# Performance work log

Measured on AMD Instinct MI355X. Metric: run time of the kernel, lower is better.

The kernel has to match this reference:

```python
import jax, jax.numpy as jnp
import numpy as np

FACTOR = 5

def setup_inputs() -> dict:
    key = jax.random.key(0)
    k1, k2, k3, k4 = jax.random.split(key, 4)
    B, L, H, D = 4, 4096, 8, 64
    sample_k = min(FACTOR * int(np.ceil(np.log(L))), L)  # 45
    queries = jax.random.normal(k1, (B, L, H, D), jnp.float32)
    keys = jax.random.normal(k2, (B, L, H, D), jnp.float32)
    values = jax.random.normal(k3, (B, L, H, D), jnp.float32)
    # torch.randint(L_K, (L_Q, sample_k)) hoisted here for determinism
    index_sample = jax.random.randint(k4, (L, sample_k), 0, L, dtype=jnp.int32)
    return {"queries": queries, "keys": keys, "values": values,
            "index_sample": index_sample}


def reference(queries, keys, values, index_sample):
    B, L_Q, H, D = queries.shape
    L_K = keys.shape[1]
    # [B,L,H,D] -> [B,H,L,D]
    Q = jnp.transpose(queries, (0, 2, 1, 3))
    K = jnp.transpose(keys, (0, 2, 1, 3))
    V = jnp.transpose(values, (0, 2, 1, 3))

    u = min(FACTOR * int(np.ceil(np.log(L_Q))), L_Q)  # n_top queries

    # --- _prob_QK: sampled QK, sparsity measure, top-u query selection ---
    # K_sample[b,h,q,s,:] = K[b,h,index_sample[q,s],:]
    K_sample = K[:, :, index_sample, :]                        # [B,H,L_Q,Sk,D]
    Q_K_sample = jnp.einsum('bhqd,bhqsd->bhqs', Q, K_sample)   # [B,H,L_Q,Sk]
    M = Q_K_sample.max(axis=-1) - Q_K_sample.sum(axis=-1) / L_K
    _, M_top = jax.lax.top_k(M, u)                             # [B,H,u]

    Q_reduce = jnp.take_along_axis(Q, M_top[..., None], axis=2)  # [B,H,u,D]
    scale = 1.0 / np.sqrt(D).astype(np.float32)
    scores = jnp.einsum('bhud,bhkd->bhuk', Q_reduce, K) * scale  # [B,H,u,L_K]

    # --- masked causal attention on the selected rows (mask_flag=True) ---
    # ProbMask: triu(1) rows gathered at M_top -> mask where col > query pos
    causal_mask = M_top[..., None] < jnp.arange(L_K)             # [B,H,u,L_K]
    scores = jnp.where(causal_mask, -jnp.inf, scores)
    attn = jax.nn.softmax(scores, axis=-1)

    # --- initial context (masked => cumsum of V), scatter top-u updates ---
    context = jnp.cumsum(V, axis=2)                              # [B,H,L_Q,D]
    update = jnp.einsum('bhuk,bhkd->bhud', attn, V)              # [B,H,u,D]
    b_idx = jnp.arange(B)[:, None, None]
    h_idx = jnp.arange(H)[None, :, None]
    context = context.at[b_idx, h_idx, M_top].set(update)
    return context  # [B,H,L_Q,D]
```

## Files before the change

### kernel.cpp

```cpp
#include <hip/hip_runtime.h>
#include <float.h>
#include <math.h>

#define B_ 4
#define L_ 4096
#define H_ 8
#define D_ 64
#define S_ 45
#define KC_ 16
#define KCH_ 256
#define SCALE 0.125f

typedef __attribute__((ext_vector_type(8))) short short8;
typedef __attribute__((ext_vector_type(4))) float float4v;

__device__ __forceinline__ ushort f2bf(float x) {
  unsigned u = __float_as_uint(x);
  return (ushort)((u + 0x7FFFu + ((u >> 16) & 1u)) >> 16);
}

__device__ __forceinline__ int swz_us(int row, int col_b, int rowb, int m) {
  int slot = (col_b >> 4) ^ (row & m);
  return row * (rowb >> 1) + (slot << 3) + ((col_b & 15) >> 1);
}

__global__ __launch_bounds__(256) void kA(
    const float* __restrict__ Q, const float* __restrict__ K,
    const float* __restrict__ V, const int* __restrict__ idxs,
    float* __restrict__ M, float* __restrict__ cs)
{
  int blk = blockIdx.x;
  int grp = blk / 136, within = blk % 136;
  int tid = threadIdx.x;
  int w = tid >> 6, lane = tid & 63;

  if (within >= 128) {
    int cblk = grp * 8 + (within - 128);
    int bh = cblk >> 4, cg = cblk & 15;
    int b = bh >> 3, h = bh & 7;
    int t = lane & 15, rg = lane >> 4;
    int c = cg * 4 + w;
    int l0 = c * 64;
    const float4* V4 = (const float4*)V;
    float4 acc = make_float4(0.f, 0.f, 0.f, 0.f);
    for (int step = 0; step < 16; ++step) {
      int l = l0 + step * 4 + rg;
      float4 v = V4[((size_t)(b * L_ + l) * H_ + h) * 16 + t];
      acc.x += v.x; acc.y += v.y; acc.z += v.z; acc.w += v.w;
    }
    acc.x += __shfl_xor(acc.x, 16, 64); acc.y += __shfl_xor(acc.y, 16, 64);
    acc.z += __shfl_xor(acc.z, 16, 64); acc.w += __shfl_xor(acc.w, 16, 64);
    acc.x += __shfl_xor(acc.x, 32, 64); acc.y += __shfl_xor(acc.y, 32, 64);
    acc.z += __shfl_xor(acc.z, 32, 64); acc.w += __shfl_xor(acc.w, 32, 64);
    if (rg == 0)
      ((float4*)cs)[((size_t)bh * 64 + c) * 16 + t] = acc;
    return;
  }

  int kblk = grp * 128 + within;
  int g = kblk & 7;
  int chunk = kblk >> 3;
  int b = g >> 1, hh = g & 1;
  int t = lane & 15;
  int l = chunk * 4 + w;

  const float4* qp = (const float4*)(Q + ((size_t)(b * L_ + l) * H_ + hh * 4) * D_);
  float4 qv = qp[lane];

  int s = lane < S_ ? lane : S_ - 1;
  int idxall = idxs[l * S_ + s];

  float vmax = -FLT_MAX, vsum = 0.f;
  #pragma unroll
  for (int c = 0; c < 5; ++c) {
    int kidx[9];
    #pragma unroll
    for (int j = 0; j < 9; ++j) kidx[j] = __shfl(idxall, c * 9 + j, 64);
    float4 kv[9];
    #pragma unroll
    for (int j = 0; j < 9; ++j) {
      const float4* kp =
          (const float4*)(K + ((size_t)(b * L_ + kidx[j]) * H_ + hh * 4) * D_);
      kv[j] = kp[lane];
    }
    #pragma unroll
    for (int j = 0; j < 9; ++j) {
      float p = qv.x * kv[j].x;
      p = fmaf(qv.y, kv[j].y, p);
      p = fmaf(qv.z, kv[j].z, p);
      p = fmaf(qv.w, kv[j].w, p);
      p += __shfl_xor(p, 1, 64);
      p += __shfl_xor(p, 2, 64);
      p += __shfl_xor(p, 4, 64);
      p += __shfl_xor(p, 8, 64);
      vmax = fmaxf(vmax, p);
      vsum += p;
    }
  }
  if (t == 0) {
    int h = hh * 4 + (lane >> 4);
    M[(size_t)(b * H_ + h) * L_ + l] = vmax - vsum * (1.0f / L_);
  }
}

__device__ __forceinline__ unsigned ordf(float f) {
  unsigned u = __float_as_uint(f);
  return (u & 0x80000000u) ? ~u : (u | 0x80000000u);
}

__global__ __launch_bounds__(256) void kB(
    const float* __restrict__ M, int* __restrict__ mtop, float* __restrict__ cs)
{
  int blk = blockIdx.x;
  int tid = threadIdx.x;
  if (blk >= 32) {
    int g = (blk - 32) * 256 + tid;
    int bh = g >> 6, d = g & 63;
    float run = 0.f;
    for (int c = 0; c < 64; ++c) {
      size_t off = ((size_t)bh * 64 + c) * D_ + d;
      float a = cs[off];
      cs[off] = run;
      run += a;
    }
    return;
  }
  __shared__ unsigned long long cand[4][S_];
  int bh = blk;
  int w = tid >> 6, lane = tid & 63;
  const float* Mp = M + (size_t)bh * L_;
  unsigned long long key[16];
  #pragma unroll
  for (int j = 0; j < 16; ++j) {
    int gi = w * 1024 + j * 64 + lane;
    key[j] = ((unsigned long long)ordf(Mp[gi]) << 32) | (unsigned)(~gi);
  }
  for (int it = 0; it < S_; ++it) {
    unsigned long long loc = key[0];
    #pragma unroll
    for (int j = 1; j < 16; ++j) loc = key[j] > loc ? key[j] : loc;
    unsigned long long best = loc;
    #pragma unroll
    for (int m = 32; m >= 1; m >>= 1) {
      unsigned long long o = __shfl_xor(best, m, 64);
      best = o > best ? o : best;
    }
    if (loc == best) {
      #pragma unroll
      for (int j = 0; j < 16; ++j) if (key[j] == best) key[j] = 0ull;
    }
    if (lane == 0) cand[w][it] = best;
  }
  __syncthreads();
  if (w == 0) {
    unsigned long long k2[3];
    #pragma unroll
    for (int j = 0; j < 3; ++j) {
      int c = j * 64 + lane;
      k2[j] = (c < 4 * S_) ? cand[c / S_][c % S_] : 0ull;
    }
    for (int it = 0; it < S_; ++it) {
      unsigned long long loc = k2[0];
      loc = k2[1] > loc ? k2[1] : loc;
      loc = k2[2] > loc ? k2[2] : loc;
      unsigned long long best = loc;
      #pragma unroll
      for (int m = 32; m >= 1; m >>= 1) {
        unsigned long long o = __shfl_xor(best, m, 64);
        best = o > best ? o : best;
      }
      if (loc == best) {
        #pragma unroll
        for (int j = 0; j < 3; ++j) if (k2[j] == best) k2[j] = 0ull;
      }
      if (lane == 0) mtop[bh * S_ + it] = (int)(~(unsigned)(best & 0xFFFFFFFFu));
    }
  }
}

__global__ __launch_bounds__(256) void kATT(
    const float* __restrict__ Q, const float* __restrict__ K,
    const float* __restrict__ V, const int* __restrict__ mtop,
    float* __restrict__ lpart, float* __restrict__ updp)
{
  __shared__ __align__(16) ushort Ks[256 * 64];
  __shared__ __align__(16) ushort Qs[48 * 64];
  __shared__ __align__(16) ushort Ps[48 * 256];
  __shared__ float lred[4][48];
  __shared__ int   cut[48];

  int blk = blockIdx.x;
  int kc = blk >> 5;
  int r5 = blk & 31;
  int bh = ((r5 & 7) << 2) | (r5 >> 3);
  int b = bh >> 3, h = bh & 7;
  int tid = threadIdx.x;
  int w = tid >> 6, lane = tid & 63;
  int l15 = lane & 15, l4 = lane >> 4;

  if (tid < 48) cut[tid] = (tid < S_) ? mtop[bh * S_ + tid] : -1;
  __syncthreads();

  {
    const float4* kp =
        (const float4*)(K + ((size_t)(b * L_ + kc * KCH_ + tid) * H_ + h) * D_);
    #pragma unroll
    for (int c = 0; c < 8; ++c) {
      float4 a = kp[2 * c], bb = kp[2 * c + 1];
      uint4 pk;
      pk.x = f2bf(a.x) | ((unsigned)f2bf(a.y) << 16);
      pk.y = f2bf(a.z) | ((unsigned)f2bf(a.w) << 16);
      pk.z = f2bf(bb.x) | ((unsigned)f2bf(bb.y) << 16);
      pk.w = f2bf(bb.z) | ((unsigned)f2bf(bb.w) << 16);
      *(uint4*)&Ks[swz_us(tid, c * 16, 128, 7)] = pk;
    }
  }
  for (int i = tid; i < 48 * 8; i += 256) {
    int row = i >> 3, c = i & 7;
    uint4 pk = make_uint4(0, 0, 0, 0);
    if (row < S_) {
      const float4* qp =
          (const float4*)(Q + ((size_t)(b * L_ + cut[row]) * H_ + h) * D_);
      float4 a = qp[2 * c], bb = qp[2 * c + 1];
      pk.x = f2bf(a.x) | ((unsigned)f2bf(a.y) << 16);
      pk.y = f2bf(a.z) | ((unsigned)f2bf(a.w) << 16);
      pk.z = f2bf(bb.x) | ((unsigned)f2bf(bb.y) << 16);
      pk.w = f2bf(bb.z) | ((unsigned)f2bf(bb.w) << 16);
    }
    *(uint4*)&Qs[swz_us(row, c * 16, 128, 7)] = pk;
  }
  __syncthreads();

  float4v accS[3][4];
  #pragma unroll
  for (int mt = 0; mt < 3; ++mt)
    #pragma unroll
    for (int nt = 0; nt < 4; ++nt)
      accS[mt][nt] = (float4v){0.f, 0.f, 0.f, 0.f};
  #pragma unroll
  for (int ks = 0; ks < 2; ++ks) {
    short8 afr[3];
    #pragma unroll
    for (int mt = 0; mt < 3; ++mt)
      afr[mt] = *(const short8*)&Qs[swz_us(mt * 16 + l15, ks * 64 + l4 * 16, 128, 7)];
    #pragma unroll
    for (int nt = 0; nt < 4; ++nt) {
      short8 bfr = *(const short8*)
          &Ks[swz_us(w * 64 + nt * 16 + l15, ks * 64 + l4 * 16, 128, 7)];
      #pragma unroll
      for (int mt = 0; mt < 3; ++mt)
        accS[mt][nt] = __builtin_amdgcn_mfma_f32_16x16x32_bf16(
            afr[mt], bfr, accS[mt][nt], 0, 0, 0);
    }
  }

  #pragma unroll
  for (int mt = 0; mt < 3; ++mt) {
    #pragma unroll
    for (int j = 0; j < 4; ++j) {
      int row = mt * 16 + l4 * 4 + j;
      int ct = cut[row];
      float rs = 0.f;
      #pragma unroll
      for (int nt = 0; nt < 4; ++nt) {
        int col = w * 64 + nt * 16 + l15;
        int kg = kc * KCH_ + col;
        float e = (kg <= ct) ? __expf(accS[mt][nt][j] * SCALE) : 0.f;
        rs += e;
        Ps[swz_us(row, col * 2, 512, 15)] = f2bf(e);
      }
      rs += __shfl_xor(rs, 1, 64);
      rs += __shfl_xor(rs, 2, 64);
      rs += __shfl_xor(rs, 4, 64);
      rs += __shfl_xor(rs, 8, 64);
      if (l15 == 0) lred[w][row] = rs;
    }
  }
  __syncthreads();

  if (tid < S_)
    lpart[((size_t)(bh * KC_ + kc)) * S_ + tid] =
        lred[0][tid] + lred[1][tid] + lred[2][tid] + lred[3][tid];

  {
    const float4* vp =
        (const float4*)(V + ((size_t)(b * L_ + kc * KCH_ + tid) * H_ + h) * D_);
    #pragma unroll
    for (int c = 0; c < 16; ++c) {
      float4 v = vp[c];
      int d0 = c * 4;
      Ks[swz_us(d0 + 0, tid * 2, 512, 15)] = f2bf(v.x);
      Ks[swz_us(d0 + 1, tid * 2, 512, 15)] = f2bf(v.y);
      Ks[swz_us(d0 + 2, tid * 2, 512, 15)] = f2bf(v.z);
      Ks[swz_us(d0 + 3, tid * 2, 512, 15)] = f2bf(v.w);
    }
  }
  __syncthreads();

  float4v accU[3];
  #pragma unroll
  for (int i = 0; i < 3; ++i) accU[i] = (float4v){0.f, 0.f, 0.f, 0.f};
  #pragma unroll
  for (int ks = 0; ks < 8; ++ks) {
    #pragma unroll
    for (int i = 0; i < 3; ++i) {
      int pi = w * 3 + i, mt = pi >> 2, nt = pi & 3;
      short8 afr = *(const short8*)
          &Ps[swz_us(mt * 16 + l15, ks * 64 + l4 * 16, 512, 15)];
      short8 bfr = *(const short8*)
          &Ks[swz_us(nt * 16 + l15, ks * 64 + l4 * 16, 512, 15)];
      accU[i] = __builtin_amdgcn_mfma_f32_16x16x32_bf16(afr, bfr, accU[i], 0, 0, 0);
    }
  }
  float* up = updp + ((size_t)(bh * KC_ + kc)) * (S_ * D_);
  #pragma unroll
  for (int i = 0; i < 3; ++i) {
    int pi = w * 3 + i, mt = pi >> 2, nt = pi & 3;
    #pragma unroll
    for (int j = 0; j < 4; ++j) {
      int row = mt * 16 + l4 * 4 + j;
      if (row < S_) up[row * D_ + nt * 16 + l15] = accU[i][j];
    }
  }
}

__global__ __launch_bounds__(256) void kW(
    const float* __restrict__ V, const float* __restrict__ cs,
    float* __restrict__ out)
{
  int blk = blockIdx.x;
  int bh = blk >> 4, cg = blk & 15;
  int b = bh >> 3, h = bh & 7;
  int w = threadIdx.x >> 6, lane = threadIdx.x & 63;
  int t = lane & 15, rg = lane >> 4;
  int c = cg * 4 + w;
  int l0 = c * 64;
  const float4* V4 = (const float4*)V;
  float4* O4 = (float4*)out;
  float4 carry = ((const float4*)cs)[((size_t)bh * 64 + c) * 16 + t];
  for (int step = 0; step < 16; ++step) {
    int l = l0 + step * 4 + rg;
    float4 v = V4[((size_t)(b * L_ + l) * H_ + h) * 16 + t];
    float4 u;
    u.x = __shfl_up(v.x, 16, 64); u.y = __shfl_up(v.y, 16, 64);
    u.z = __shfl_up(v.z, 16, 64); u.w = __shfl_up(v.w, 16, 64);
    if (rg >= 1) { v.x += u.x; v.y += u.y; v.z += u.z; v.w += u.w; }
    u.x = __shfl_up(v.x, 32, 64); u.y = __shfl_up(v.y, 32, 64);
    u.z = __shfl_up(v.z, 32, 64); u.w = __shfl_up(v.w, 32, 64);
    if (rg >= 2) { v.x += u.x; v.y += u.y; v.z += u.z; v.w += u.w; }
    float4 o;
    o.x = carry.x + v.x; o.y = carry.y + v.y;
    o.z = carry.z + v.z; o.w = carry.w + v.w;
    O4[((size_t)bh * L_ + l) * 16 + t] = o;
    carry.x += __shfl(v.x, 48 + t, 64); carry.y += __shfl(v.y, 48 + t, 64);
    carry.z += __shfl(v.z, 48 + t, 64); carry.w += __shfl(v.w, 48 + t, 64);
  }
}

__global__ __launch_bounds__(256) void kD(
    const float* __restrict__ lpart, const float* __restrict__ updp,
    const int* __restrict__ mtop, float* __restrict__ out)
{
  __shared__ float linv[S_];
  __shared__ int   mt[S_];
  int bh = blockIdx.x;
  int tid = threadIdx.x;
  if (tid < S_) {
    float l = 0.f;
    for (int kc = 0; kc < KC_; ++kc) l += lpart[(size_t)(bh * KC_ + kc) * S_ + tid];
    linv[tid] = 1.0f / l;
    mt[tid] = mtop[bh * S_ + tid];
  }
  __syncthreads();
  for (int i = tid; i < S_ * D_; i += 256) {
    int r = i >> 6, d = i & 63;
    float u = 0.f;
    for (int kc = 0; kc < KC_; ++kc) u += updp[((size_t)(bh * KC_ + kc)) * (S_ * D_) + i];
    out[((size_t)bh * L_ + mt[r]) * D_ + d] = u * linv[r];
  }
}

extern "C" void kernel_launch(void* const* d_in, const int* in_sizes, int n_in,
                              void* d_out, int out_size, void* d_ws, size_t ws_size,
                              hipStream_t stream) {
  const float* Q = (const float*)d_in[0];
  const float* K = (const float*)d_in[1];
  const float* V = (const float*)d_in[2];
  const int*   I = (const int*)d_in[3];
  float* out = (float*)d_out;
  float* ws = (float*)d_ws;

  float* M     = ws;
  float* cs    = ws + 131072;
  float* lpart = ws + 262144;
  float* updp  = ws + 262144 + 23040;
  int*   mtop  = (int*)(ws + 262144 + 23040 + 1474560);

  kA<<<64 * 136, 256, 0, stream>>>(Q, K, V, I, M, cs);
  kB<<<40, 256, 0, stream>>>(M, mtop, cs);
  kATT<<<B_ * H_ * KC_, 256, 0, stream>>>(Q, K, V, mtop, lpart, updp);
  kW<<<B_ * H_ * 16, 256, 0, stream>>>(V, cs, out);
  kD<<<B_ * H_, 256, 0, stream>>>(lpart, updp, mtop, out);
}
```

Baseline: 188.0 us.

## Fuse cumsum writer into attention kernel and halve key chunk size

Merges the cumsum-writer kernel into the attention kernel as extra block roles, interleaving 8 writer blocks with 16 attention blocks per group. It also halves the key chunk to 128, doubling the attention blocks to 1024 and using less shared memory each. The kB prefix scan now loads its 64 values into registers before writing them back. The aim is more parallelism and occupancy and one fewer launch, at the cost of twice the partial sums, so kD does more reduction work.

```diff
diff --git a/kernel.cpp b/kernel.cpp
--- a/kernel.cpp
+++ b/kernel.cpp
@@ -7,8 +7,8 @@
 #define H_ 8
 #define D_ 64
 #define S_ 45
-#define KC_ 16
-#define KCH_ 256
+#define KC2_ 32
+#define KCH2_ 128
 #define SCALE 0.125f
 
 typedef __attribute__((ext_vector_type(8))) short short8;
@@ -116,11 +116,14 @@
   if (blk >= 32) {
     int g = (blk - 32) * 256 + tid;
     int bh = g >> 6, d = g & 63;
+    float v[64];
+    #pragma unroll
+    for (int c = 0; c < 64; ++c) v[c] = cs[((size_t)bh * 64 + c) * D_ + d];
     float run = 0.f;
+    #pragma unroll
     for (int c = 0; c < 64; ++c) {
-      size_t off = ((size_t)bh * 64 + c) * D_ + d;
-      float a = cs[off];
-      cs[off] = run;
+      float a = v[c];
+      cs[((size_t)bh * 64 + c) * D_ + d] = run;
       run += a;
     }
     return;
@@ -178,41 +181,77 @@
   }
 }
 
-__global__ __launch_bounds__(256) void kATT(
+__global__ __launch_bounds__(256) void kCW(
     const float* __restrict__ Q, const float* __restrict__ K,
-    const float* __restrict__ V, const int* __restrict__ mtop,
-    float* __restrict__ lpart, float* __restrict__ updp)
+    const float* __restrict__ V, const float* __restrict__ cs,
+    const int* __restrict__ mtop, float* __restrict__ lpart,
+    float* __restrict__ updp, float* __restrict__ out)
 {
-  __shared__ __align__(16) ushort Ks[256 * 64];
+  __shared__ __align__(16) ushort Ks[128 * 64];
   __shared__ __align__(16) ushort Qs[48 * 64];
-  __shared__ __align__(16) ushort Ps[48 * 256];
+  __shared__ __align__(16) ushort Ps[48 * 128];
   __shared__ float lred[4][48];
   __shared__ int   cut[48];
 
   int blk = blockIdx.x;
-  int kc = blk >> 5;
-  int r5 = blk & 31;
+  int grp = blk / 24, within = blk % 24;
+  int tid = threadIdx.x;
+  int w = tid >> 6, lane = tid & 63;
+
+  if (within >= 16) {
+    int wblk = grp * 8 + (within - 16);
+    int bh = wblk >> 4, cg = wblk & 15;
+    int b = bh >> 3, h = bh & 7;
+    int t = lane & 15, rg = lane >> 4;
+    int c = cg * 4 + w;
+    int l0 = c * 64;
+    const float4* V4 = (const float4*)V;
+    float4* O4 = (float4*)out;
+    float4 carry = ((const float4*)cs)[((size_t)bh * 64 + c) * 16 + t];
+    for (int step = 0; step < 16; ++step) {
+      int l = l0 + step * 4 + rg;
+      float4 v = V4[((size_t)(b * L_ + l) * H_ + h) * 16 + t];
+      float4 u;
+      u.x = __shfl_up(v.x, 16, 64); u.y = __shfl_up(v.y, 16, 64);
+      u.z = __shfl_up(v.z, 16, 64); u.w = __shfl_up(v.w, 16, 64);
+      if (rg >= 1) { v.x += u.x; v.y += u.y; v.z += u.z; v.w += u.w; }
+      u.x = __shfl_up(v.x, 32, 64); u.y = __shfl_up(v.y, 32, 64);
+      u.z = __shfl_up(v.z, 32, 64); u.w = __shfl_up(v.w, 32, 64);
+      if (rg >= 2) { v.x += u.x; v.y += u.y; v.z += u.z; v.w += u.w; }
+      float4 o;
+      o.x = carry.x + v.x; o.y = carry.y + v.y;
+      o.z = carry.z + v.z; o.w = carry.w + v.w;
+      O4[((size_t)bh * L_ + l) * 16 + t] = o;
+      carry.x += __shfl(v.x, 48 + t, 64); carry.y += __shfl(v.y, 48 + t, 64);
+      carry.z += __shfl(v.z, 48 + t, 64); carry.w += __shfl(v.w, 48 + t, 64);
+    }
+    return;
+  }
+
+  int ablk = grp * 16 + within;
+  int kc = ablk >> 5;
+  int r5 = ablk & 31;
   int bh = ((r5 & 7) << 2) | (r5 >> 3);
   int b = bh >> 3, h = bh & 7;
-  int tid = threadIdx.x;
-  int w = tid >> 6, lane = tid & 63;
   int l15 = lane & 15, l4 = lane >> 4;
 
   if (tid < 48) cut[tid] = (tid < S_) ? mtop[bh * S_ + tid] : -1;
   __syncthreads();
 
   {
+    int row = tid & 127, half = tid >> 7;
     const float4* kp =
-        (const float4*)(K + ((size_t)(b * L_ + kc * KCH_ + tid) * H_ + h) * D_);
-    #pragma unroll
-    for (int c = 0; c < 8; ++c) {
+        (const float4*)(K + ((size_t)(b * L_ + kc * KCH2_ + row) * H_ + h) * D_);
+    #pragma unroll
+    for (int cc = 0; cc < 4; ++cc) {
+      int c = half * 4 + cc;
       float4 a = kp[2 * c], bb = kp[2 * c + 1];
       uint4 pk;
       pk.x = f2bf(a.x) | ((unsigned)f2bf(a.y) << 16);
       pk.y = f2bf(a.z) | ((unsigned)f2bf(a.w) << 16);
       pk.z = f2bf(bb.x) | ((unsigned)f2bf(bb.y) << 16);
       pk.w = f2bf(bb.z) | ((unsigned)f2bf(bb.w) << 16);
-      *(uint4*)&Ks[swz_us(tid, c * 16, 128, 7)] = pk;
+      *(uint4*)&Ks[swz_us(row, c * 16, 128, 7)] = pk;
     }
   }
   for (int i = tid; i < 48 * 8; i += 256) {
@@ -231,11 +270,11 @@
   }
   __syncthreads();
 
-  float4v accS[3][4];
+  float4v accS[3][2];
   #pragma unroll
   for (int mt = 0; mt < 3; ++mt)
     #pragma unroll
-    for (int nt = 0; nt < 4; ++nt)
+    for (int nt = 0; nt < 2; ++nt)
       accS[mt][nt] = (float4v){0.f, 0.f, 0.f, 0.f};
   #pragma unroll
   for (int ks = 0; ks < 2; ++ks) {
@@ -244,9 +283,9 @@
     for (int mt = 0; mt < 3; ++mt)
       afr[mt] = *(const short8*)&Qs[swz_us(mt * 16 + l15, ks * 64 + l4 * 16, 128, 7)];
     #pragma unroll
-    for (int nt = 0; nt < 4; ++nt) {
+    for (int nt = 0; nt < 2; ++nt) {
       short8 bfr = *(const short8*)
-          &Ks[swz_us(w * 64 + nt * 16 + l15, ks * 64 + l4 * 16, 128, 7)];
+          &Ks[swz_us(w * 32 + nt * 16 + l15, ks * 64 + l4 * 16, 128, 7)];
       #pragma unroll
       for (int mt = 0; mt < 3; ++mt)
         accS[mt][nt] = __builtin_amdgcn_mfma_f32_16x16x32_bf16(
@@ -262,12 +301,12 @@
       int ct = cut[row];
       float rs = 0.f;
       #pragma unroll
-      for (int nt = 0; nt < 4; ++nt) {
-        int col = w * 64 + nt * 16 + l15;
-        int kg = kc * KCH_ + col;
+      for (int nt = 0; nt < 2; ++nt) {
+        int col = w * 32 + nt * 16 + l15;
+        int kg = kc * KCH2_ + col;
         float e = (kg <= ct) ? __expf(accS[mt][nt][j] * SCALE) : 0.f;
         rs += e;
-        Ps[swz_us(row, col * 2, 512, 15)] = f2bf(e);
+        Ps[swz_us(row, col * 2, 256, 15)] = f2bf(e);
       }
       rs += __shfl_xor(rs, 1, 64);
       rs += __shfl_xor(rs, 2, 64);
@@ -279,20 +318,22 @@
   __syncthreads();
 
   if (tid < S_)
-    lpart[((size_t)(bh * KC_ + kc)) * S_ + tid] =
+    lpart[((size_t)(bh * KC2_ + kc)) * S_ + tid] =
         lred[0][tid] + lred[1][tid] + lred[2][tid] + lred[3][tid];
 
   {
+    int row = tid & 127, half = tid >> 7;
     const float4* vp =
-        (const float4*)(V + ((size_t)(b * L_ + kc * KCH_ + tid) * H_ + h) * D_);
-    #pragma unroll
-    for (int c = 0; c < 16; ++c) {
+        (const float4*)(V + ((size_t)(b * L_ + kc * KCH2_ + row) * H_ + h) * D_);
+    #pragma unroll
+    for (int cc = 0; cc < 8; ++cc) {
+      int c = half * 8 + cc;
       float4 v = vp[c];
       int d0 = c * 4;
-      Ks[swz_us(d0 + 0, tid * 2, 512, 15)] = f2bf(v.x);
-      Ks[swz_us(d0 + 1, tid * 2, 512, 15)] = f2bf(v.y);
-      Ks[swz_us(d0 + 2, tid * 2, 512, 15)] = f2bf(v.z);
-      Ks[swz_us(d0 + 3, tid * 2, 512, 15)] = f2bf(v.w);
+      Ks[swz_us(d0 + 0, row * 2, 256, 15)] = f2bf(v.x);
+      Ks[swz_us(d0 + 1, row * 2, 256, 15)] = f2bf(v.y);
+      Ks[swz_us(d0 + 2, row * 2, 256, 15)] = f2bf(v.z);
+      Ks[swz_us(d0 + 3, row * 2, 256, 15)] = f2bf(v.w);
     }
   }
   __syncthreads();
@@ -301,18 +342,18 @@
   #pragma unroll
   for (int i = 0; i < 3; ++i) accU[i] = (float4v){0.f, 0.f, 0.f, 0.f};
   #pragma unroll
-  for (int ks = 0; ks < 8; ++ks) {
+  for (int ks = 0; ks < 4; ++ks) {
     #pragma unroll
     for (int i = 0; i < 3; ++i) {
       int pi = w * 3 + i, mt = pi >> 2, nt = pi & 3;
       short8 afr = *(const short8*)
-          &Ps[swz_us(mt * 16 + l15, ks * 64 + l4 * 16, 512, 15)];
+          &Ps[swz_us(mt * 16 + l15, ks * 64 + l4 * 16, 256, 15)];
       short8 bfr = *(const short8*)
-          &Ks[swz_us(nt * 16 + l15, ks * 64 + l4 * 16, 512, 15)];
+          &Ks[swz_us(nt * 16 + l15, ks * 64 + l4 * 16, 256, 15)];
       accU[i] = __builtin_amdgcn_mfma_f32_16x16x32_bf16(afr, bfr, accU[i], 0, 0, 0);
     }
   }
-  float* up = updp + ((size_t)(bh * KC_ + kc)) * (S_ * D_);
+  float* up = updp + ((size_t)(bh * KC2_ + kc)) * (S_ * D_);
   #pragma unroll
   for (int i = 0; i < 3; ++i) {
     int pi = w * 3 + i, mt = pi >> 2, nt = pi & 3;
@@ -321,39 +362,6 @@
       int row = mt * 16 + l4 * 4 + j;
       if (row < S_) up[row * D_ + nt * 16 + l15] = accU[i][j];
     }
-  }
-}
-
-__global__ __launch_bounds__(256) void kW(
-    const float* __restrict__ V, const float* __restrict__ cs,
-    float* __restrict__ out)
-{
-  int blk = blockIdx.x;
-  int bh = blk >> 4, cg = blk & 15;
-  int b = bh >> 3, h = bh & 7;
-  int w = threadIdx.x >> 6, lane = threadIdx.x & 63;
-  int t = lane & 15, rg = lane >> 4;
-  int c = cg * 4 + w;
-  int l0 = c * 64;
-  const float4* V4 = (const float4*)V;
-  float4* O4 = (float4*)out;
-  float4 carry = ((const float4*)cs)[((size_t)bh * 64 + c) * 16 + t];
-  for (int step = 0; step < 16; ++step) {
-    int l = l0 + step * 4 + rg;
-    float4 v = V4[((size_t)(b * L_ + l) * H_ + h) * 16 + t];
-    float4 u;
-    u.x = __shfl_up(v.x, 16, 64); u.y = __shfl_up(v.y, 16, 64);
-    u.z = __shfl_up(v.z, 16, 64); u.w = __shfl_up(v.w, 16, 64);
-    if (rg >= 1) { v.x += u.x; v.y += u.y; v.z += u.z; v.w += u.w; }
-    u.x = __shfl_up(v.x, 32, 64); u.y = __shfl_up(v.y, 32, 64);
-    u.z = __shfl_up(v.z, 32, 64); u.w = __shfl_up(v.w, 32, 64);
-    if (rg >= 2) { v.x += u.x; v.y += u.y; v.z += u.z; v.w += u.w; }
-    float4 o;
-    o.x = carry.x + v.x; o.y = carry.y + v.y;
-    o.z = carry.z + v.z; o.w = carry.w + v.w;
-    O4[((size_t)bh * L_ + l) * 16 + t] = o;
-    carry.x += __shfl(v.x, 48 + t, 64); carry.y += __shfl(v.y, 48 + t, 64);
-    carry.z += __shfl(v.z, 48 + t, 64); carry.w += __shfl(v.w, 48 + t, 64);
   }
 }
 
@@ -367,7 +375,7 @@
   int tid = threadIdx.x;
   if (tid < S_) {
     float l = 0.f;
-    for (int kc = 0; kc < KC_; ++kc) l += lpart[(size_t)(bh * KC_ + kc) * S_ + tid];
+    for (int kc = 0; kc < KC2_; ++kc) l += lpart[(size_t)(bh * KC2_ + kc) * S_ + tid];
     linv[tid] = 1.0f / l;
     mt[tid] = mtop[bh * S_ + tid];
   }
@@ -375,7 +383,7 @@
   for (int i = tid; i < S_ * D_; i += 256) {
     int r = i >> 6, d = i & 63;
     float u = 0.f;
-    for (int kc = 0; kc < KC_; ++kc) u += updp[((size_t)(bh * KC_ + kc)) * (S_ * D_) + i];
+    for (int kc = 0; kc < KC2_; ++kc) u += updp[((size_t)(bh * KC2_ + kc)) * (S_ * D_) + i];
     out[((size_t)bh * L_ + mt[r]) * D_ + d] = u * linv[r];
   }
 }
@@ -393,12 +401,11 @@
   float* M     = ws;
   float* cs    = ws + 131072;
   float* lpart = ws + 262144;
-  float* updp  = ws + 262144 + 23040;
-  int*   mtop  = (int*)(ws + 262144 + 23040 + 1474560);
+  float* updp  = ws + 308224;
+  int*   mtop  = (int*)(ws + 308224 + 2949120);
 
   kA<<<64 * 136, 256, 0, stream>>>(Q, K, V, I, M, cs);
   kB<<<40, 256, 0, stream>>>(M, mtop, cs);
-  kATT<<<B_ * H_ * KC_, 256, 0, stream>>>(Q, K, V, mtop, lpart, updp);
-  kW<<<B_ * H_ * 16, 256, 0, stream>>>(V, cs, out);
+  kCW<<<64 * 24, 256, 0, stream>>>(Q, K, V, cs, mtop, lpart, updp, out);
   kD<<<B_ * H_, 256, 0, stream>>>(lpart, updp, mtop, out);
 }
```

Result: slower. 200.7 us (+6.8%).

## Split sampled-QK work across half-waves, fuse cumsum write with scatter kernel

Applied to the files above, without the earlier changes.

The sampled QK kernel now gives each wave two heads instead of four, with the two 32-lane halves handling alternate samples, and doubles the grid in two batch phases to raise parallelism and memory-level concurrency. The cumsum-carry prefix in kB is register-buffered and unrolled. The cumsum writer and the top-u scatter kernel are merged into one launch, using a shared-memory bitmask so cumsum rows that will be overwritten by the scatter are skipped. This removes a kernel launch and avoids write races between the two blocks, at the cost of extra shuffles and an atomic bitmask setup per block.

```diff
diff --git a/kernel.cpp b/kernel.cpp
--- a/kernel.cpp
+++ b/kernel.cpp
@@ -35,6 +35,7 @@
   int w = tid >> 6, lane = tid & 63;
 
   if (within >= 128) {
+    if (grp >= 64) return;
     int cblk = grp * 8 + (within - 128);
     int bh = cblk >> 4, cg = cblk & 15;
     int b = bh >> 3, h = bh & 7;
@@ -58,37 +59,41 @@
   }
 
   int kblk = grp * 128 + within;
-  int g = kblk & 7;
-  int chunk = kblk >> 3;
-  int b = g >> 1, hh = g & 1;
-  int t = lane & 15;
+  int phase = kblk >> 13;
+  int pblk = kblk & 8191;
+  int g = pblk & 7;
+  int b = (g >> 2) + phase * 2;
+  int hq = g & 3;
+  int chunk = pblk >> 3;
   int l = chunk * 4 + w;
-
-  const float4* qp = (const float4*)(Q + ((size_t)(b * L_ + l) * H_ + hh * 4) * D_);
-  float4 qv = qp[lane];
+  int t31 = lane & 31;
+  int half = lane >> 5;
+
+  const float4* qp =
+      (const float4*)(Q + ((size_t)(b * L_ + l) * H_ + hq * 2) * D_);
+  float4 qv = qp[t31];
 
   int s = lane < S_ ? lane : S_ - 1;
   int idxall = idxs[l * S_ + s];
 
   float vmax = -FLT_MAX, vsum = 0.f;
   #pragma unroll
-  for (int c = 0; c < 5; ++c) {
-    int kidx[9];
-    #pragma unroll
-    for (int j = 0; j < 9; ++j) kidx[j] = __shfl(idxall, c * 9 + j, 64);
-    float4 kv[9];
-    #pragma unroll
-    for (int j = 0; j < 9; ++j) {
-      const float4* kp =
-          (const float4*)(K + ((size_t)(b * L_ + kidx[j]) * H_ + hh * 4) * D_);
-      kv[j] = kp[lane];
-    }
-    #pragma unroll
-    for (int j = 0; j < 9; ++j) {
-      float p = qv.x * kv[j].x;
-      p = fmaf(qv.y, kv[j].y, p);
-      p = fmaf(qv.z, kv[j].z, p);
-      p = fmaf(qv.w, kv[j].w, p);
+  for (int c = 0; c < 3; ++c) {
+    int kidx[6];
+    #pragma unroll
+    for (int jj = 0; jj < 6; ++jj)
+      kidx[jj] = __shfl(idxall, (c * 6 + jj) * 2 + half, 64);
+    float4 kv[6];
+    #pragma unroll
+    for (int jj = 0; jj < 6; ++jj)
+      kv[jj] = ((const float4*)(K +
+          ((size_t)(b * L_ + kidx[jj]) * H_ + hq * 2) * D_))[t31];
+    #pragma unroll
+    for (int jj = 0; jj < 6; ++jj) {
+      float p = qv.x * kv[jj].x;
+      p = fmaf(qv.y, kv[jj].y, p);
+      p = fmaf(qv.z, kv[jj].z, p);
+      p = fmaf(qv.w, kv[jj].w, p);
       p += __shfl_xor(p, 1, 64);
       p += __shfl_xor(p, 2, 64);
       p += __shfl_xor(p, 4, 64);
@@ -97,8 +102,37 @@
       vsum += p;
     }
   }
-  if (t == 0) {
-    int h = hh * 4 + (lane >> 4);
+  {
+    int kidx[5];
+    #pragma unroll
+    for (int jj = 0; jj < 5; ++jj) {
+      int s2 = (18 + jj) * 2 + half;
+      kidx[jj] = __shfl(idxall, s2 > 44 ? 44 : s2, 64);
+    }
+    float4 kv[5];
+    #pragma unroll
+    for (int jj = 0; jj < 5; ++jj)
+      kv[jj] = ((const float4*)(K +
+          ((size_t)(b * L_ + kidx[jj]) * H_ + hq * 2) * D_))[t31];
+    #pragma unroll
+    for (int jj = 0; jj < 5; ++jj) {
+      float p = qv.x * kv[jj].x;
+      p = fmaf(qv.y, kv[jj].y, p);
+      p = fmaf(qv.z, kv[jj].z, p);
+      p = fmaf(qv.w, kv[jj].w, p);
+      p += __shfl_xor(p, 1, 64);
+      p += __shfl_xor(p, 2, 64);
+      p += __shfl_xor(p, 4, 64);
+      p += __shfl_xor(p, 8, 64);
+      bool dup = (jj == 4) && (half == 1);
+      vmax = fmaxf(vmax, p);
+      if (!dup) vsum += p;
+    }
+  }
+  vmax = fmaxf(vmax, __shfl_xor(vmax, 32, 64));
+  vsum += __shfl_xor(vsum, 32, 64);
+  if ((lane & 15) == 0 && half == 0) {
+    int h = hq * 2 + (lane >> 4);
     M[(size_t)(b * H_ + h) * L_ + l] = vmax - vsum * (1.0f / L_);
   }
 }
@@ -116,11 +150,14 @@
   if (blk >= 32) {
     int g = (blk - 32) * 256 + tid;
     int bh = g >> 6, d = g & 63;
+    float v[64];
+    #pragma unroll
+    for (int c = 0; c < 64; ++c) v[c] = cs[((size_t)bh * 64 + c) * D_ + d];
     float run = 0.f;
+    #pragma unroll
     for (int c = 0; c < 64; ++c) {
-      size_t off = ((size_t)bh * 64 + c) * D_ + d;
-      float a = cs[off];
-      cs[off] = run;
+      float a = v[c];
+      cs[((size_t)bh * 64 + c) * D_ + d] = run;
       run += a;
     }
     return;
@@ -324,14 +361,48 @@
   }
 }
 
-__global__ __launch_bounds__(256) void kW(
+__global__ __launch_bounds__(256) void kWD(
     const float* __restrict__ V, const float* __restrict__ cs,
-    float* __restrict__ out)
+    const float* __restrict__ lpart, const float* __restrict__ updp,
+    const int* __restrict__ mtop, float* __restrict__ out)
 {
   int blk = blockIdx.x;
+  int tid = threadIdx.x;
+
+  if (blk >= 512) {
+    __shared__ float linv[S_];
+    __shared__ int   mt[S_];
+    int bh = blk - 512;
+    if (tid < S_) {
+      float l = 0.f;
+      for (int kc = 0; kc < KC_; ++kc) l += lpart[(size_t)(bh * KC_ + kc) * S_ + tid];
+      linv[tid] = 1.0f / l;
+      mt[tid] = mtop[bh * S_ + tid];
+    }
+    __syncthreads();
+    for (int i = tid; i < S_ * D_; i += 256) {
+      int r = i >> 6, d = i & 63;
+      float u = 0.f;
+      for (int kc = 0; kc < KC_; ++kc)
+        u += updp[((size_t)(bh * KC_ + kc)) * (S_ * D_) + i];
+      out[((size_t)bh * L_ + mt[r]) * D_ + d] = u * linv[r];
+    }
+    return;
+  }
+
+  __shared__ unsigned bits[8];
   int bh = blk >> 4, cg = blk & 15;
+  int base = cg * 256;
+  if (tid < 8) bits[tid] = 0u;
+  __syncthreads();
+  if (tid < S_) {
+    int r = mtop[bh * S_ + tid] - base;
+    if ((unsigned)r < 256u) atomicOr(&bits[r >> 5], 1u << (r & 31));
+  }
+  __syncthreads();
+
   int b = bh >> 3, h = bh & 7;
-  int w = threadIdx.x >> 6, lane = threadIdx.x & 63;
+  int w = tid >> 6, lane = tid & 63;
   int t = lane & 15, rg = lane >> 4;
   int c = cg * 4 + w;
   int l0 = c * 64;
@@ -348,35 +419,15 @@
     u.x = __shfl_up(v.x, 32, 64); u.y = __shfl_up(v.y, 32, 64);
     u.z = __shfl_up(v.z, 32, 64); u.w = __shfl_up(v.w, 32, 64);
     if (rg >= 2) { v.x += u.x; v.y += u.y; v.z += u.z; v.w += u.w; }
-    float4 o;
-    o.x = carry.x + v.x; o.y = carry.y + v.y;
-    o.z = carry.z + v.z; o.w = carry.w + v.w;
-    O4[((size_t)bh * L_ + l) * 16 + t] = o;
+    int wl = l - base;
+    if (!((bits[wl >> 5] >> (wl & 31)) & 1u)) {
+      float4 o;
+      o.x = carry.x + v.x; o.y = carry.y + v.y;
+      o.z = carry.z + v.z; o.w = carry.w + v.w;
+      O4[((size_t)bh * L_ + l) * 16 + t] = o;
+    }
     carry.x += __shfl(v.x, 48 + t, 64); carry.y += __shfl(v.y, 48 + t, 64);
     carry.z += __shfl(v.z, 48 + t, 64); carry.w += __shfl(v.w, 48 + t, 64);
-  }
-}
-
-__global__ __launch_bounds__(256) void kD(
-    const float* __restrict__ lpart, const float* __restrict__ updp,
-    const int* __restrict__ mtop, float* __restrict__ out)
-{
-  __shared__ float linv[S_];
-  __shared__ int   mt[S_];
-  int bh = blockIdx.x;
-  int tid = threadIdx.x;
-  if (tid < S_) {
-    float l = 0.f;
-    for (int kc = 0; kc < KC_; ++kc) l += lpart[(size_t)(bh * KC_ + kc) * S_ + tid];
-    linv[tid] = 1.0f / l;
-    mt[tid] = mtop[bh * S_ + tid];
-  }
-  __syncthreads();
-  for (int i = tid; i < S_ * D_; i += 256) {
-    int r = i >> 6, d = i & 63;
-    float u = 0.f;
-    for (int kc = 0; kc < KC_; ++kc) u += updp[((size_t)(bh * KC_ + kc)) * (S_ * D_) + i];
-    out[((size_t)bh * L_ + mt[r]) * D_ + d] = u * linv[r];
   }
 }
 
@@ -396,9 +447,8 @@
   float* updp  = ws + 262144 + 23040;
   int*   mtop  = (int*)(ws + 262144 + 23040 + 1474560);
 
-  kA<<<64 * 136, 256, 0, stream>>>(Q, K, V, I, M, cs);
+  kA<<<128 * 136, 256, 0, stream>>>(Q, K, V, I, M, cs);
   kB<<<40, 256, 0, stream>>>(M, mtop, cs);
   kATT<<<B_ * H_ * KC_, 256, 0, stream>>>(Q, K, V, mtop, lpart, updp);
-  kW<<<B_ * H_ * 16, 256, 0, stream>>>(V, cs, out);
-  kD<<<B_ * H_, 256, 0, stream>>>(lpart, updp, mtop, out);
-}
+  kWD<<<544, 256, 0, stream>>>(V, cs, lpart, updp, mtop, out);
+}
```

Measured after the change: 174.9 us. 1.07x faster.
